# Performance work log

Measured on AMD Instinct MI355X. Metric: run time of the kernel, lower is better.

The kernel has to match this reference:

```python
import jax, jax.numpy as jnp
import numpy as np

LATENT = 256
M_FEAT = 17
B, L = 512, 512
IN_SZ = M_FEAT + LATENT  # 273


def setup_inputs() -> dict:
    key = jax.random.key(0)
    ks = jax.random.split(key, 9)
    k = 1.0 / np.sqrt(LATENT)  # pytorch LSTM/Linear init scale
    u = lambda kk, shape, s: jax.random.uniform(kk, shape, jnp.float32, -s, s)
    return {
        "in_sequence": jax.random.normal(ks[0], (B, L, LATENT), jnp.float32),
        "h0": jax.random.normal(ks[1], (1, B, LATENT), jnp.float32),
        "c0": jax.random.normal(ks[2], (1, B, LATENT), jnp.float32),
        "W_ih": u(ks[3], (4 * LATENT, IN_SZ), k),
        "W_hh": u(ks[4], (4 * LATENT, LATENT), k),
        "b_ih": u(ks[5], (4 * LATENT,), k),
        "b_hh": u(ks[6], (4 * LATENT,), k),
        "W_lin": u(ks[7], (M_FEAT, LATENT), 1.0 / np.sqrt(LATENT)),
        "b_lin": u(ks[8], (M_FEAT,), 1.0 / np.sqrt(LATENT)),
    }


def reference(in_sequence, h0, c0, W_ih, W_hh, b_ih, b_hh, W_lin, b_lin):
    Bb, Ll, H = in_sequence.shape
    Mf = W_lin.shape[0]
    b = b_ih + b_hh
    xs = jnp.swapaxes(in_sequence, 0, 1)  # (L, B, H)

    def step(carry, z):
        h, c, out_prev = carry
        x_t = jnp.concatenate([out_prev, z], axis=-1)  # (B, M+H)
        gates = x_t @ W_ih.T + h @ W_hh.T + b  # (B, 4H), gate order i,f,g,o
        i_g, f_g, g_g, o_g = jnp.split(gates, 4, axis=-1)
        c_new = jax.nn.sigmoid(f_g) * c + jax.nn.sigmoid(i_g) * jnp.tanh(g_g)
        h_new = jax.nn.sigmoid(o_g) * jnp.tanh(c_new)
        out = h_new @ W_lin.T + b_lin  # (B, M)
        return (h_new, c_new, out), out

    out0 = jnp.zeros((Bb, Mf), in_sequence.dtype)  # start token
    _, outs = jax.lax.scan(step, (h0[0], c0[0], out0), xs)
    return jnp.swapaxes(outs, 0, 1)  # (B, L, M)
```

## Files before the change

### kernel.cpp

```cpp
#include <hip/hip_runtime.h>

#define BATCH 512
#define SEQL  512
#define HID   256
#define MF    17
#define G4    1024
#define KX    512
#define PBLK  16
#define NGRP  16
#define BG    32
#define NTHR  512

#define WS_WC  ((size_t)0)
#define WS_BC  (WS_WC + (size_t)G4*KX)
#define WS_C0  (WS_BC + (size_t)G4)
#define WS_HB  (WS_C0 + (size_t)BATCH*G4)
#define WS_CNT (WS_HB + (size_t)2*BATCH*HID)
#define WS_END (WS_CNT + 1024)

#define WLPAD  516
#define L_WL   0
#define L_XS   (64*WLPAD)
#define L_GS   L_XS
#define L_HST  (L_XS + 2*32*68)
#define LDS_FLOATS (L_HST + 16*33)
#define LDS_BYTES  (LDS_FLOATS*4)

__global__ void k_fold(const float* __restrict__ Wih, const float* __restrict__ Whh,
                       const float* __restrict__ bih, const float* __restrict__ bhh,
                       const float* __restrict__ Wlin, const float* __restrict__ blin,
                       float* __restrict__ ws)
{
    int r = blockIdx.x;
    int g = r >> 8;
    int u = r & 255;
    int s = u >> 4;
    int rho = s*64 + g*16 + (u & 15);
    __shared__ float wrow[17];
    int tid = threadIdx.x;
    if (tid < 17) wrow[tid] = Wih[(size_t)r*273 + tid];
    __syncthreads();
    float* Wc = ws + WS_WC + (size_t)rho*KX;
    for (int k = tid; k < KX; k += 128) {
        float v;
        if (k < 256) {
            v = Wih[(size_t)r*273 + 17 + k];
        } else {
            int kk = k - 256;
            v = Whh[(size_t)r*256 + kk];
            #pragma unroll
            for (int m = 0; m < 17; ++m) v += wrow[m]*Wlin[m*256 + kk];
        }
        Wc[k] = v;
    }
    if (tid == 0) {
        float b = bih[r] + bhh[r];
        #pragma unroll
        for (int m = 0; m < 17; ++m) b += wrow[m]*blin[m];
        ws[WS_BC + rho] = b;
    }
}

__global__ void k_c0(const float* __restrict__ Wih, const float* __restrict__ Wlin,
                     const float* __restrict__ blin, const float* __restrict__ h0,
                     float* __restrict__ ws)
{
    int b = blockIdx.x;
    int tid = threadIdx.x;
    __shared__ float part[17][8];
    __shared__ float t0[17];
    if (tid < 136) {
        int m = tid >> 3, p = tid & 7;
        const float* h = h0 + (size_t)b*256;
        float sacc = 0.f;
        for (int k = p*32; k < p*32 + 32; ++k) sacc += Wlin[m*256 + k]*h[k];
        part[m][p] = sacc;
    }
    __syncthreads();
    if (tid < 17) {
        float sacc = blin[tid];
        #pragma unroll
        for (int p = 0; p < 8; ++p) sacc += part[tid][p];
        t0[tid] = sacc;
    }
    __syncthreads();
    for (int rho = tid; rho < G4; rho += 256) {
        int s_ = rho >> 6;
        int g  = (rho >> 4) & 3;
        int ul = rho & 15;
        int r  = g*256 + s_*16 + ul;
        float v = 0.f;
        #pragma unroll
        for (int m = 0; m < 17; ++m) v += Wih[(size_t)r*273 + m]*t0[m];
        ws[WS_C0 + (size_t)b*G4 + rho] = v;
    }
}

__global__ void __launch_bounds__(NTHR) k_lstm(
    const float* __restrict__ inseq, const float* __restrict__ h0,
    const float* __restrict__ c0,   const float* __restrict__ Wlin,
    const float* __restrict__ blin, float* __restrict__ ws,
    float* __restrict__ out)
{
    extern __shared__ float lds[];
    float* Wl  = lds + L_WL;
    float* xsb = lds + L_XS;
    float* Gs  = lds + L_GS;
    float* hst = lds + L_HST;

    const int bid = blockIdx.x;
    const int xcd = bid & 7, j = bid >> 3;
    const int gg  = xcd + 8*(j >> 4);
    const int s   = j & 15;
    const int tid = threadIdx.x;

    {
        int row = tid >> 3, seg = tid & 7;
        const float* src = ws + WS_WC + (size_t)(s*64 + row)*KX + seg*64;
        float* dst = Wl + row*WLPAD + seg*64;
        #pragma unroll
        for (int i = 0; i < 64; i += 4)
            *(float4*)(dst + i) = *(const float4*)(src + i);
    }

    const int uu = tid >> 5;
    const int ub = tid & 31;
    float bc4[4], c04[4];
    #pragma unroll
    for (int g = 0; g < 4; ++g) bc4[g] = ws[WS_BC + s*64 + g*16 + uu];
    #pragma unroll
    for (int g = 0; g < 4; ++g) c04[g] = ws[WS_C0 + (size_t)(gg*32 + ub)*G4 + s*64 + g*16 + uu];
    float creg = c0[(size_t)(gg*32 + ub)*256 + s*16 + uu];

    const int bb = tid >> 4;
    const int kq = tid & 15;
    float4 wl1[4], wl2[4];
    #pragma unroll
    for (int cc = 0; cc < 4; ++cc) {
        int kh = cc*64 + 4*kq;
        wl1[cc] = *(const float4*)(Wlin + s*256 + kh);
        if (s == 0) wl2[cc] = *(const float4*)(Wlin + 16*256 + kh);
        else        wl2[cc] = make_float4(0.f,0.f,0.f,0.f);
    }

    const int rg = tid >> 4;
    const int bp = tid & 15;
    const float* wrow0 = Wl + (2*rg)*WLPAD;
    const float* wrow1 = Wl + (2*rg + 1)*WLPAD;

    int* cnt = (int*)(ws + WS_CNT) + gg*32;
    const float* zbase = inseq + (size_t)(gg*32)*SEQL*HID;
    float* hb = ws + WS_HB;

    float oacc1 = 0.f, oacc2 = 0.f;
    __syncthreads();

    for (int t = 0; t < SEQL; ++t) {
        const float* hsrc = (t == 0)
            ? (h0 + (size_t)(gg*32)*HID)
            : (hb + (size_t)((t & 1) ^ 1)*BATCH*HID + (size_t)(gg*32)*HID);

        {
            float4 v = *(const float4*)(zbase + (size_t)bb*SEQL*HID + (size_t)t*HID + 4*kq);
            *(float4*)(xsb + bb*68 + 4*kq) = v;
        }
        __syncthreads();

        float a00 = 0.f, a01 = 0.f, a10 = 0.f, a11 = 0.f;
        #pragma unroll
        for (int c = 0; c < 8; ++c) {
            if (c < 7) {
                const int cn = c + 1;
                float* xbn = xsb + (cn & 1)*(32*68);
                float4 v;
                if (cn < 4) {
                    v = *(const float4*)(zbase + (size_t)bb*SEQL*HID + (size_t)t*HID + cn*64 + 4*kq);
                } else {
                    v = *(const float4*)(hsrc + (size_t)bb*HID + (cn - 4)*64 + 4*kq);
                    const int cc = cn - 4;
                    oacc1 += v.x*wl1[cc].x + v.y*wl1[cc].y + v.z*wl1[cc].z + v.w*wl1[cc].w;
                    if (s == 0)
                        oacc2 += v.x*wl2[cc].x + v.y*wl2[cc].y + v.z*wl2[cc].z + v.w*wl2[cc].w;
                }
                *(float4*)(xbn + bb*68 + 4*kq) = v;
            }
            {
                const float* xbc = xsb + (c & 1)*(32*68);
                const float* w0 = wrow0 + c*64;
                const float* w1 = wrow1 + c*64;
                const float* x0p = xbc + bp*68;
                const float* x1p = xbc + (bp + 16)*68;
                #pragma unroll
                for (int k = 0; k < 64; k += 4) {
                    float4 wa = *(const float4*)(w0 + k);
                    float4 wb = *(const float4*)(w1 + k);
                    float4 x0 = *(const float4*)(x0p + k);
                    float4 x1 = *(const float4*)(x1p + k);
                    a00 = fmaf(wa.x,x0.x, fmaf(wa.y,x0.y, fmaf(wa.z,x0.z, fmaf(wa.w,x0.w, a00))));
                    a01 = fmaf(wa.x,x1.x, fmaf(wa.y,x1.y, fmaf(wa.z,x1.z, fmaf(wa.w,x1.w, a01))));
                    a10 = fmaf(wb.x,x0.x, fmaf(wb.y,x0.y, fmaf(wb.z,x0.z, fmaf(wb.w,x0.w, a10))));
                    a11 = fmaf(wb.x,x1.x, fmaf(wb.y,x1.y, fmaf(wb.z,x1.z, fmaf(wb.w,x1.w, a11))));
                }
            }
            __syncthreads();
        }

        {
            float r1 = oacc1, r2 = oacc2;
            #pragma unroll
            for (int off = 8; off; off >>= 1) {
                r1 += __shfl_xor(r1, off, 16);
                if (s == 0) r2 += __shfl_xor(r2, off, 16);
            }
            if (t > 0 && kq == 0) {
                float* o = out + ((size_t)(gg*32 + bb)*SEQL + (t - 1))*MF;
                o[s] = r1 + blin[s];
                if (s == 0) o[16] = r2 + blin[16];
            }
            oacc1 = 0.f; oacc2 = 0.f;
        }

        Gs[(2*rg)*33 + bp]        = a00;
        Gs[(2*rg)*33 + bp + 16]   = a01;
        Gs[(2*rg + 1)*33 + bp]      = a10;
        Gs[(2*rg + 1)*33 + bp + 16] = a11;
        __syncthreads();

        {
            float ig = Gs[(  0 + uu)*33 + ub] + bc4[0];
            float fg = Gs[( 16 + uu)*33 + ub] + bc4[1];
            float gv = Gs[( 32 + uu)*33 + ub] + bc4[2];
            float og = Gs[( 48 + uu)*33 + ub] + bc4[3];
            if (t == 0) { ig -= c04[0]; fg -= c04[1]; gv -= c04[2]; og -= c04[3]; }
            float si = 1.f/(1.f + __expf(-ig));
            float sf = 1.f/(1.f + __expf(-fg));
            float so = 1.f/(1.f + __expf(-og));
            float tg = tanhf(gv);
            creg = sf*creg + si*tg;
            float h = so*tanhf(creg);
            hst[uu*33 + ub] = h;
        }
        __syncthreads();

        {
            int b2 = tid >> 4, u2 = tid & 15;
            hb[(size_t)(t & 1)*BATCH*HID + (size_t)(gg*32 + b2)*HID + s*16 + u2] = hst[u2*33 + b2];
        }
        __syncthreads();

        if (tid == 0) {
            __builtin_amdgcn_fence(__ATOMIC_RELEASE, "agent");
            __hip_atomic_fetch_add(cnt, 1, __ATOMIC_RELAXED, __HIP_MEMORY_SCOPE_AGENT);
            const int target = PBLK*(t + 1);
            while (__hip_atomic_load(cnt, __ATOMIC_RELAXED, __HIP_MEMORY_SCOPE_AGENT) < target)
                __builtin_amdgcn_s_sleep(2);
            __builtin_amdgcn_fence(__ATOMIC_ACQUIRE, "agent");
        }
        __syncthreads();
    }

    {
        const float* hfin = hb + (size_t)1*BATCH*HID + (size_t)(gg*32)*HID;
        float r1 = 0.f, r2 = 0.f;
        #pragma unroll
        for (int cc = 0; cc < 4; ++cc) {
            float4 v = *(const float4*)(hfin + (size_t)bb*HID + cc*64 + 4*kq);
            r1 += v.x*wl1[cc].x + v.y*wl1[cc].y + v.z*wl1[cc].z + v.w*wl1[cc].w;
            if (s == 0)
                r2 += v.x*wl2[cc].x + v.y*wl2[cc].y + v.z*wl2[cc].z + v.w*wl2[cc].w;
        }
        #pragma unroll
        for (int off = 8; off; off >>= 1) {
            r1 += __shfl_xor(r1, off, 16);
            r2 += __shfl_xor(r2, off, 16);
        }
        if (kq == 0) {
            float* o = out + ((size_t)(gg*32 + bb)*SEQL + (SEQL - 1))*MF;
            o[s] = r1 + blin[s];
            if (s == 0) o[16] = r2 + blin[16];
        }
    }
}

extern "C" void kernel_launch(void* const* d_in, const int* in_sizes, int n_in,
                              void* d_out, int out_size, void* d_ws, size_t ws_size,
                              hipStream_t stream)
{
    const float* inseq = (const float*)d_in[0];
    const float* h0    = (const float*)d_in[1];
    const float* c0    = (const float*)d_in[2];
    const float* Wih   = (const float*)d_in[3];
    const float* Whh   = (const float*)d_in[4];
    const float* bih   = (const float*)d_in[5];
    const float* bhh   = (const float*)d_in[6];
    const float* Wlin  = (const float*)d_in[7];
    const float* blin  = (const float*)d_in[8];
    float* outp = (float*)d_out;
    float* ws   = (float*)d_ws;

    static bool attr_set = false;
    if (!attr_set) {
        hipFuncSetAttribute((const void*)k_lstm,
                            hipFuncAttributeMaxDynamicSharedMemorySize, LDS_BYTES);
        attr_set = true;
    }

    hipMemsetAsync((char*)d_ws + WS_CNT*sizeof(float), 0, 1024*sizeof(int), stream);

    k_fold<<<dim3(G4), dim3(128), 0, stream>>>(Wih, Whh, bih, bhh, Wlin, blin, ws);
    k_c0  <<<dim3(BATCH), dim3(256), 0, stream>>>(Wih, Wlin, blin, h0, ws);

    void* fp_in  = (void*)inseq; void* fp_h0 = (void*)h0; void* fp_c0 = (void*)c0;
    void* fp_wl  = (void*)Wlin;  void* fp_bl = (void*)blin;
    void* fp_ws  = (void*)ws;    void* fp_o  = (void*)outp;
    void* args[7] = { &fp_in, &fp_h0, &fp_c0, &fp_wl, &fp_bl, &fp_ws, &fp_o };
    hipLaunchCooperativeKernel((const void*)k_lstm, dim3(256), dim3(NTHR),
                               args, LDS_BYTES, stream);
}
```

Before: 230.0 ms.

## Use 4x4 register tiling with split-K shuffles and drop fences in grid barrier

Each thread now computes a 4x4 register tile of gate rows by batch over a quarter of each 16-wide K slice, then reduces across 4 lanes with shuffles. This replaces the old 2x2 tile and raises FMA-to-LDS-load ratio; the weight padding changes to reduce bank conflicts. The per-step barrier drops the release/acquire fences in favor of relaxed atomic loads/stores on the hidden-state buffer and adds a spin guard, which reduces sync cost but weakens memory-ordering guarantees and could time out silently.

```diff
diff --git a/kernel.cpp b/kernel.cpp
--- a/kernel.cpp
+++ b/kernel.cpp
@@ -18,13 +18,17 @@
 #define WS_CNT (WS_HB + (size_t)2*BATCH*HID)
 #define WS_END (WS_CNT + 1024)
 
-#define WLPAD  516
+#define WLPAD  517
+#define XPAD   68
 #define L_WL   0
 #define L_XS   (64*WLPAD)
 #define L_GS   L_XS
-#define L_HST  (L_XS + 2*32*68)
+#define L_HST  (L_XS + 2*32*XPAD)
 #define LDS_FLOATS (L_HST + 16*33)
 #define LDS_BYTES  (LDS_FLOATS*4)
+
+#define AT_LD(p)    __hip_atomic_load((p), __ATOMIC_RELAXED, __HIP_MEMORY_SCOPE_AGENT)
+#define AT_ST(p, v) __hip_atomic_store((p), (v), __ATOMIC_RELAXED, __HIP_MEMORY_SCOPE_AGENT)
 
 __global__ void k_fold(const float* __restrict__ Wih, const float* __restrict__ Whh,
                        const float* __restrict__ bih, const float* __restrict__ bhh,
@@ -143,10 +147,9 @@
         else        wl2[cc] = make_float4(0.f,0.f,0.f,0.f);
     }
 
-    const int rg = tid >> 4;
-    const int bp = tid & 15;
-    const float* wrow0 = Wl + (2*rg)*WLPAD;
-    const float* wrow1 = Wl + (2*rg + 1)*WLPAD;
+    const int ks = tid & 3;
+    const int bq = (tid >> 2) & 7;
+    const int rq = tid >> 5;
 
     int* cnt = (int*)(ws + WS_CNT) + gg*32;
     const float* zbase = inseq + (size_t)(gg*32)*SEQL*HID;
@@ -162,44 +165,58 @@
 
         {
             float4 v = *(const float4*)(zbase + (size_t)bb*SEQL*HID + (size_t)t*HID + 4*kq);
-            *(float4*)(xsb + bb*68 + 4*kq) = v;
-        }
-        __syncthreads();
-
-        float a00 = 0.f, a01 = 0.f, a10 = 0.f, a11 = 0.f;
+            *(float4*)(xsb + bb*XPAD + 4*kq) = v;
+        }
+        __syncthreads();
+
+        float acc[4][4];
+        #pragma unroll
+        for (int i = 0; i < 4; ++i)
+            #pragma unroll
+            for (int jj = 0; jj < 4; ++jj) acc[i][jj] = 0.f;
+
         #pragma unroll
         for (int c = 0; c < 8; ++c) {
             if (c < 7) {
                 const int cn = c + 1;
-                float* xbn = xsb + (cn & 1)*(32*68);
+                float* xbn = xsb + (cn & 1)*(32*XPAD);
                 float4 v;
                 if (cn < 4) {
                     v = *(const float4*)(zbase + (size_t)bb*SEQL*HID + (size_t)t*HID + cn*64 + 4*kq);
                 } else {
-                    v = *(const float4*)(hsrc + (size_t)bb*HID + (cn - 4)*64 + 4*kq);
+                    const float* hp = hsrc + (size_t)bb*HID + (cn - 4)*64 + 4*kq;
+                    v.x = AT_LD(hp + 0);
+                    v.y = AT_LD(hp + 1);
+                    v.z = AT_LD(hp + 2);
+                    v.w = AT_LD(hp + 3);
                     const int cc = cn - 4;
                     oacc1 += v.x*wl1[cc].x + v.y*wl1[cc].y + v.z*wl1[cc].z + v.w*wl1[cc].w;
                     if (s == 0)
                         oacc2 += v.x*wl2[cc].x + v.y*wl2[cc].y + v.z*wl2[cc].z + v.w*wl2[cc].w;
                 }
-                *(float4*)(xbn + bb*68 + 4*kq) = v;
+                *(float4*)(xbn + bb*XPAD + 4*kq) = v;
             }
             {
-                const float* xbc = xsb + (c & 1)*(32*68);
-                const float* w0 = wrow0 + c*64;
-                const float* w1 = wrow1 + c*64;
-                const float* x0p = xbc + bp*68;
-                const float* x1p = xbc + (bp + 16)*68;
+                const float* xbc = xsb + (c & 1)*(32*XPAD);
                 #pragma unroll
-                for (int k = 0; k < 64; k += 4) {
-                    float4 wa = *(const float4*)(w0 + k);
-                    float4 wb = *(const float4*)(w1 + k);
-                    float4 x0 = *(const float4*)(x0p + k);
-                    float4 x1 = *(const float4*)(x1p + k);
-                    a00 = fmaf(wa.x,x0.x, fmaf(wa.y,x0.y, fmaf(wa.z,x0.z, fmaf(wa.w,x0.w, a00))));
-                    a01 = fmaf(wa.x,x1.x, fmaf(wa.y,x1.y, fmaf(wa.z,x1.z, fmaf(wa.w,x1.w, a01))));
-                    a10 = fmaf(wb.x,x0.x, fmaf(wb.y,x0.y, fmaf(wb.z,x0.z, fmaf(wb.w,x0.w, a10))));
-                    a11 = fmaf(wb.x,x1.x, fmaf(wb.y,x1.y, fmaf(wb.z,x1.z, fmaf(wb.w,x1.w, a11))));
+                for (int g2 = 0; g2 < 4; ++g2) {
+                    const int ko = c*64 + g2*16 + ks*4;
+                    const int xo = g2*16 + ks*4;
+                    float4 wv[4], xv[4];
+                    #pragma unroll
+                    for (int i = 0; i < 4; ++i)
+                        wv[i] = *(const float4*)(Wl + (4*rq + i)*WLPAD + ko);
+                    #pragma unroll
+                    for (int jj = 0; jj < 4; ++jj)
+                        xv[jj] = *(const float4*)(xbc + (4*bq + jj)*XPAD + xo);
+                    #pragma unroll
+                    for (int i = 0; i < 4; ++i)
+                        #pragma unroll
+                        for (int jj = 0; jj < 4; ++jj)
+                            acc[i][jj] = fmaf(wv[i].x, xv[jj].x,
+                                         fmaf(wv[i].y, xv[jj].y,
+                                         fmaf(wv[i].z, xv[jj].z,
+                                         fmaf(wv[i].w, xv[jj].w, acc[i][jj]))));
                 }
             }
             __syncthreads();
@@ -220,10 +237,15 @@
             oacc1 = 0.f; oacc2 = 0.f;
         }
 
-        Gs[(2*rg)*33 + bp]        = a00;
-        Gs[(2*rg)*33 + bp + 16]   = a01;
-        Gs[(2*rg + 1)*33 + bp]      = a10;
-        Gs[(2*rg + 1)*33 + bp + 16] = a11;
+        #pragma unroll
+        for (int i = 0; i < 4; ++i)
+            #pragma unroll
+            for (int jj = 0; jj < 4; ++jj) {
+                float v = acc[i][jj];
+                v += __shfl_xor(v, 1);
+                v += __shfl_xor(v, 2);
+                if (ks == 0) Gs[(4*rq + i)*33 + 4*bq + jj] = v;
+            }
         __syncthreads();
 
         {
@@ -244,17 +266,20 @@
 
         {
             int b2 = tid >> 4, u2 = tid & 15;
-            hb[(size_t)(t & 1)*BATCH*HID + (size_t)(gg*32 + b2)*HID + s*16 + u2] = hst[u2*33 + b2];
+            AT_ST(hb + (size_t)(t & 1)*BATCH*HID + (size_t)(gg*32 + b2)*HID + s*16 + u2,
+                  hst[u2*33 + b2]);
         }
         __syncthreads();
 
         if (tid == 0) {
-            __builtin_amdgcn_fence(__ATOMIC_RELEASE, "agent");
             __hip_atomic_fetch_add(cnt, 1, __ATOMIC_RELAXED, __HIP_MEMORY_SCOPE_AGENT);
             const int target = PBLK*(t + 1);
-            while (__hip_atomic_load(cnt, __ATOMIC_RELAXED, __HIP_MEMORY_SCOPE_AGENT) < target)
+            int guard = 0;
+            while (__hip_atomic_load(cnt, __ATOMIC_RELAXED, __HIP_MEMORY_SCOPE_AGENT) < target
+                   && guard < (1 << 16)) {
                 __builtin_amdgcn_s_sleep(2);
-            __builtin_amdgcn_fence(__ATOMIC_ACQUIRE, "agent");
+                ++guard;
+            }
         }
         __syncthreads();
     }
@@ -264,7 +289,12 @@
         float r1 = 0.f, r2 = 0.f;
         #pragma unroll
         for (int cc = 0; cc < 4; ++cc) {
-            float4 v = *(const float4*)(hfin + (size_t)bb*HID + cc*64 + 4*kq);
+            const float* hp = hfin + (size_t)bb*HID + cc*64 + 4*kq;
+            float4 v;
+            v.x = AT_LD(hp + 0);
+            v.y = AT_LD(hp + 1);
+            v.z = AT_LD(hp + 2);
+            v.w = AT_LD(hp + 3);
             r1 += v.x*wl1[cc].x + v.y*wl1[cc].y + v.z*wl1[cc].z + v.w*wl1[cc].w;
             if (s == 0)
                 r2 += v.x*wl2[cc].x + v.y*wl2[cc].y + v.z*wl2[cc].z + v.w*wl2[cc].w;
```

New measurement: 203.1 ms. 1.13x faster.
